# Kernel optimization log

Hardware: AMD Instinct MI355X
Metric: run time of the kernel (lower is better)

The kernel has to match this reference:

```python
import jax, jax.numpy as jnp
import numpy as np

N, K, FEAT = 64, 32, 1024      # nodes, neighbors per node, input feature dim
C1, F1 = 4, 16                 # layer1: out_channels=4, out_features=hidden[0]/4=16
C2, F2 = 32, 1                 # layer2: out_channels=hidden[1]=32, out_features=1
NUM_CLASS = 10
BN_EPS = 1e-5


def _sgnroot(x):
    return jnp.sign(x) * jnp.sqrt(jnp.clip(jnp.abs(x), 1e-8))


def _feature_adjacency(x, nb):
    # x: (N,c,f), nb: (N,K,c,f) -> adj: (N,c,f,f)
    fadj = jnp.einsum('nca,nkcb->ncab', x, nb)          # sum over K neighbors
    fadj = fadj + jnp.swapaxes(fadj, -2, -1)
    s = _sgnroot(fadj)
    out = s / (jnp.abs(s).sum(axis=1, keepdims=True) + 1e-7)  # row-normalize over channel dim
    return jnp.where(jnp.isnan(out), 0.0, out)


def _layer(x, nb, W, c_out, f_out):
    # FeatTrans1d.forward: adjacency build + batched matmul + full-width conv (== dense contraction)
    n = x.shape[0]
    adj = _feature_adjacency(x, nb)                     # (N,c,f,f)
    xa = jnp.einsum('ncab,ncb->nca', adj, x)            # adj @ x
    x2 = jnp.einsum('ocf,ncf->no', W, xa).reshape(n, c_out, f_out)
    na = jnp.einsum('ncab,nkcb->nkca', adj, nb)         # per-node adj applied to its neighbors
    nb2 = jnp.einsum('ocf,nkcf->nko', W, na).reshape(n, -1, c_out, f_out)
    return x2, nb2


def _bn_softsign_x(x, w, b):
    # BatchNorm1d (training stats over batch+feature dims) + Softsign; x: (N,C,F)
    m = x.mean(axis=(0, 2), keepdims=True)
    v = x.var(axis=(0, 2), keepdims=True)
    y = (x - m) / jnp.sqrt(v + BN_EPS) * w[None, :, None] + b[None, :, None]
    return y / (1.0 + jnp.abs(y))


def _bn_softsign_nb(x, w, b):
    # each node's neighbor set is normalized independently (list comprehension in original); x: (N,K,C,F)
    m = x.mean(axis=(1, 3), keepdims=True)
    v = x.var(axis=(1, 3), keepdims=True)
    y = (x - m) / jnp.sqrt(v + BN_EPS) * w[None, None, :, None] + b[None, None, :, None]
    return y / (1.0 + jnp.abs(y))


def setup_inputs() -> dict:
    key = jax.random.key(0)
    ks = jax.random.split(key, 6)
    return {
        'x': jax.random.normal(ks[0], (N, 1, FEAT), jnp.float32),
        'neighbor': jax.random.normal(ks[1], (N, K, 1, FEAT), jnp.float32),
        'W1': jax.random.normal(ks[2], (C1 * F1, 1, FEAT), jnp.float32) * (1.0 / FEAT) ** 0.5,
        'W2': jax.random.normal(ks[3], (C2 * F2, C1, F1), jnp.float32) * (1.0 / (C1 * F1)) ** 0.5,
        'bn1_w': jnp.ones((C1,), jnp.float32),
        'bn1_b': jnp.zeros((C1,), jnp.float32),
        'bn2_w': jnp.ones((C2,), jnp.float32),
        'bn2_b': jnp.zeros((C2,), jnp.float32),
        'lin_w': jax.random.normal(ks[4], (NUM_CLASS, C2 * F2), jnp.float32) * (1.0 / (C2 * F2)) ** 0.5,
        'lin_b': jnp.zeros((NUM_CLASS,), jnp.float32),
    }


def reference(x, neighbor, W1, W2, bn1_w, bn1_b, bn2_w, bn2_b, lin_w, lin_b):
    x1, nb1 = _layer(x, neighbor, W1, C1, F1)           # (N,4,16), (N,K,4,16)
    x1 = _bn_softsign_x(x1, bn1_w, bn1_b)
    nb1 = _bn_softsign_nb(nb1, bn1_w, bn1_b)
    x2, _ = _layer(x1, nb1, W2, C2, F2)                 # (N,32,1)
    x2 = _bn_softsign_x(x2, bn2_w, bn2_b)
    return x2.reshape(x2.shape[0], -1) @ lin_w.T + lin_b  # (N,NUM_CLASS)
```

## Files before the change

kernel.cpp:

```cpp
#include <hip/hip_runtime.h>

typedef unsigned short u16;
typedef short short8 __attribute__((ext_vector_type(8)));
typedef float floatx4 __attribute__((ext_vector_type(4)));
typedef float floatx2 __attribute__((ext_vector_type(2)));
typedef unsigned int uintx4 __attribute__((ext_vector_type(4)));
typedef unsigned int uintx2 __attribute__((ext_vector_type(2)));
typedef u16 ushortx4 __attribute__((ext_vector_type(4)));

#define FEAT 1024
#define KNB  32

__device__ __forceinline__ u16 f2bf(float f) {
    unsigned u = __float_as_uint(f);
    u += 0x7fffu + ((u >> 16) & 1u);
    return (u16)(u >> 16);
}
__device__ __forceinline__ unsigned pack2bf(float a, float b) {
    return (unsigned)f2bf(a) | ((unsigned)f2bf(b) << 16);
}
__device__ __forceinline__ float softsign(float v) { return v / (1.f + fabsf(v)); }

union Frag { uintx4 q; unsigned d[4]; short8 v; };

union SMem {
    struct {
        float sS[FEAT];
        float sX[FEAT];
        u16   sY[34 * 1024];
    } p1;
    struct {
        float sx2[64 * 64];
        float snb[32 * 64];
        float sx1[64], sS1[64], sadj[4 * 16 * 16], sxa[64];
        float ssc[4], sbi[4], ssc2[4], sbi2[4];
        int   flag;
    } p2;
    struct {
        float sy[64 * 32];
        float sx[64 * 32];
        float ssc[32], sbi[32];
    } p3;
};

__global__ __launch_bounds__(256, 2) void k_mega(
    const float* __restrict__ xg, const float* __restrict__ nbg,
    const float* __restrict__ w1g, const float* __restrict__ w2g,
    const float* __restrict__ bn1w, const float* __restrict__ bn1b,
    const float* __restrict__ bn2w, const float* __restrict__ bn2b,
    const float* __restrict__ linw, const float* __restrict__ linb,
    float* __restrict__ pws, float* __restrict__ x22ws,
    unsigned int* __restrict__ cnt, float* __restrict__ outg)
{
    __shared__ SMem sm;
    float* const sS = sm.p1.sS;
    float* const sX = sm.p1.sX;
    u16*   const sY = sm.p1.sY;

    const int t = threadIdx.x;
    const int bid = blockIdx.x;
    const int n = bid >> 3;
    const int chunk = bid & 7;
    const int chunkbase = chunk * 128;
    const int w = t >> 6;
    const int l = t & 63;
    const int m = l & 15;
    const int g = l >> 4;

    {
        ushortx4 z4 = {0, 0, 0, 0};
        *(ushortx4*)&sY[33 * 1024 + t * 4] = z4;
    }
    {
        floatx4 xv = *(const floatx4*)(xg + (size_t)n * FEAT + t * 4);
        *(floatx4*)&sX[t * 4] = xv;
        ushortx4 xb4 = {f2bf(xv[0]), f2bf(xv[1]), f2bf(xv[2]), f2bf(xv[3])};
        *(ushortx4*)&sY[t * 4] = xb4;
    }
    {
        const float* nbase = nbg + ((size_t)n * KNB) * FEAT + t * 4;
        floatx4 sacc = {0.f, 0.f, 0.f, 0.f};
        #pragma unroll 8
        for (int k = 0; k < KNB; ++k) {
            floatx4 v = *(const floatx4*)(nbase + (size_t)k * FEAT);
            sacc += v;
            int row = k + 1;
            int c16 = (t >> 1) ^ (row & 7);
            ushortx4 p4 = {f2bf(v[0]), f2bf(v[1]), f2bf(v[2]), f2bf(v[3])};
            *(ushortx4*)&sY[row * 1024 + c16 * 8 + (t & 1) * 4] = p4;
        }
        *(floatx4*)&sS[t * 4] = sacc;
    }

    const float xa0 = xg[(size_t)n * FEAT + chunkbase + w * 32 + m];
    const float xa1 = xg[(size_t)n * FEAT + chunkbase + w * 32 + 16 + m];
    __syncthreads();
    const float Sa0 = sS[chunkbase + w * 32 + m];
    const float Sa1 = sS[chunkbase + w * 32 + 16 + m];

    const u16* b2base = (m == 0) ? &sY[32 * 1024] : &sY[33 * 1024];
    const int sw = (m & 7);

    floatx4 acc[2][3];
    #pragma unroll
    for (int i = 0; i < 2; ++i)
        #pragma unroll
        for (int j = 0; j < 3; ++j) { floatx4 z = {0.f, 0.f, 0.f, 0.f}; acc[i][j] = z; }

    const floatx2 vxa0 = {xa0, xa0}, vxa1 = {xa1, xa1};
    const floatx2 vSa0 = {Sa0, Sa0}, vSa1 = {Sa1, Sa1};

    #pragma unroll 2
    for (int s = 0; s < 32; ++s) {
        const int bloc = s * 32 + g * 8;
        const int cidx = bloc >> 3;

        floatx4 xq0 = *(const floatx4*)&sX[bloc];
        floatx4 xq1 = *(const floatx4*)&sX[bloc + 4];
        floatx4 sq0 = *(const floatx4*)&sS[bloc];
        floatx4 sq1 = *(const floatx4*)&sS[bloc + 4];

        Frag af0, af1;
        #pragma unroll
        for (int p = 0; p < 4; ++p) {
            floatx2 xbp = (p < 2) ? ((p == 0) ? (floatx2){xq0[0], xq0[1]} : (floatx2){xq0[2], xq0[3]})
                                  : ((p == 2) ? (floatx2){xq1[0], xq1[1]} : (floatx2){xq1[2], xq1[3]});
            floatx2 sbp = (p < 2) ? ((p == 0) ? (floatx2){sq0[0], sq0[1]} : (floatx2){sq0[2], sq0[3]})
                                  : ((p == 2) ? (floatx2){sq1[0], sq1[1]} : (floatx2){sq1[2], sq1[3]});
            floatx2 u0 = xbp * vSa0 + sbp * vxa0;
            floatx2 u1 = xbp * vSa1 + sbp * vxa1;
            uintx2 b0b = __builtin_bit_cast(uintx2, u0);
            uintx2 b1b = __builtin_bit_cast(uintx2, u1);
            af0.d[p] = 0x3F803F80u | (b0b.y & 0x80000000u) | ((b0b.x >> 16) & 0x8000u);
            af1.d[p] = 0x3F803F80u | (b1b.y & 0x80000000u) | ((b1b.x >> 16) & 0x8000u);
        }

        Frag b0, b1, b2;
        b0.q = *(const uintx4*)&sY[ m       * 1024 + ((cidx ^ sw) << 3)];
        b1.q = *(const uintx4*)&sY[(16 + m) * 1024 + ((cidx ^ sw) << 3)];
        b2.q = *(const uintx4*)&b2base[cidx << 3];

        acc[0][0] = __builtin_amdgcn_mfma_f32_16x16x32_bf16(af0.v, b0.v, acc[0][0], 0, 0, 0);
        acc[0][1] = __builtin_amdgcn_mfma_f32_16x16x32_bf16(af0.v, b1.v, acc[0][1], 0, 0, 0);
        acc[0][2] = __builtin_amdgcn_mfma_f32_16x16x32_bf16(af0.v, b2.v, acc[0][2], 0, 0, 0);
        acc[1][0] = __builtin_amdgcn_mfma_f32_16x16x32_bf16(af1.v, b0.v, acc[1][0], 0, 0, 0);
        acc[1][1] = __builtin_amdgcn_mfma_f32_16x16x32_bf16(af1.v, b1.v, acc[1][1], 0, 0, 0);
        acc[1][2] = __builtin_amdgcn_mfma_f32_16x16x32_bf16(af1.v, b2.v, acc[1][2], 0, 0, 0);
    }
    __syncthreads();

    u16* sZ = sY;
    #pragma unroll
    for (int ti = 0; ti < 2; ++ti)
        #pragma unroll
        for (int jt = 0; jt < 3; ++jt) {
            int j = jt * 16 + m;
            int aloc = w * 32 + ti * 16 + g * 4;
            ushortx4 zz;
            zz.x = f2bf(acc[ti][jt][0]);
            zz.y = f2bf(acc[ti][jt][1]);
            zz.z = f2bf(acc[ti][jt][2]);
            zz.w = f2bf(acc[ti][jt][3]);
            *(ushortx4*)&sZ[j * 136 + aloc] = zz;
        }
    __syncthreads();

    floatx4 a2[3];
    #pragma unroll
    for (int j = 0; j < 3; ++j) { floatx4 z = {0.f, 0.f, 0.f, 0.f}; a2[j] = z; }
    #pragma unroll
    for (int kc = 0; kc < 4; ++kc) {
        const float* wsrc = w1g + (size_t)(w * 16 + m) * FEAT + chunkbase + kc * 32 + g * 8;
        floatx4 wf0 = *(const floatx4*)wsrc;
        floatx4 wf1 = *(const floatx4*)(wsrc + 4);
        Frag wb;
        wb.d[0] = pack2bf(wf0[0], wf0[1]);
        wb.d[1] = pack2bf(wf0[2], wf0[3]);
        wb.d[2] = pack2bf(wf1[0], wf1[1]);
        wb.d[3] = pack2bf(wf1[2], wf1[3]);
        #pragma unroll
        for (int jt = 0; jt < 3; ++jt) {
            Frag za;
            za.q = *(const uintx4*)&sZ[(jt * 16 + m) * 136 + kc * 32 + g * 8];
            a2[jt] = __builtin_amdgcn_mfma_f32_16x16x32_bf16(za.v, wb.v, a2[jt], 0, 0, 0);
        }
    }
    float* pbase = pws + (size_t)(n * 8 + chunk) * 33 * 64;
    #pragma unroll
    for (int jt = 0; jt < 3; ++jt)
        #pragma unroll
        for (int r = 0; r < 4; ++r) {
            int j = jt * 16 + g * 4 + r;
            if (j < 33)
                __hip_atomic_store(&pbase[j * 64 + w * 16 + m], a2[jt][r],
                                   __ATOMIC_RELAXED, __HIP_MEMORY_SCOPE_AGENT);
        }

    asm volatile("s_waitcnt vmcnt(0)" ::: "memory");
    __syncthreads();
    if (t == 0)
        __hip_atomic_fetch_add(&cnt[0], 1u, __ATOMIC_RELAXED, __HIP_MEMORY_SCOPE_AGENT);

    if ((bid & 7) != (n & 7)) return;

    if (t == 0) {
        while (__hip_atomic_load(&cnt[0], __ATOMIC_RELAXED, __HIP_MEMORY_SCOPE_AGENT) < 512u)
            __builtin_amdgcn_s_sleep(8);
    }
    __syncthreads();

    float* const sx2  = sm.p2.sx2;
    float* const snb  = sm.p2.snb;
    float* const sx1  = sm.p2.sx1;
    float* const sS1  = sm.p2.sS1;
    float* const sadj = sm.p2.sadj;
    float* const sxa  = sm.p2.sxa;
    float* const ssc  = sm.p2.ssc;
    float* const sbi  = sm.p2.sbi;
    float* const ssc2 = sm.p2.ssc2;
    float* const sbi2 = sm.p2.sbi2;

    #pragma unroll
    for (int r = 0; r < 4; ++r) {
        int slot = t + r * 256;
        int nn = slot >> 4, oc = slot & 15;
        const float* p = pws + (size_t)nn * 16896 + oc * 4;
        floatx4 tmp[8];
        #pragma unroll
        for (int c = 0; c < 8; ++c) tmp[c] = *(const floatx4*)(p + c * 2112);
        floatx4 s01 = tmp[0] + tmp[1], s23 = tmp[2] + tmp[3];
        floatx4 s45 = tmp[4] + tmp[5], s67 = tmp[6] + tmp[7];
        *(floatx4*)&sx2[slot * 4] = (s01 + s23) + (s45 + s67);
    }
    #pragma unroll
    for (int r = 0; r < 2; ++r) {
        int slot = t + r * 256;
        int k = slot >> 4, oc = slot & 15;
        const float* p = pws + (size_t)n * 16896 + (1 + k) * 64 + oc * 4;
        floatx4 tmp[8];
        #pragma unroll
        for (int c = 0; c < 8; ++c) tmp[c] = *(const floatx4*)(p + c * 2112);
        floatx4 s01 = tmp[0] + tmp[1], s23 = tmp[2] + tmp[3];
        floatx4 s45 = tmp[4] + tmp[5], s67 = tmp[6] + tmp[7];
        *(floatx4*)&snb[slot * 4] = (s01 + s23) + (s45 + s67);
    }
    __syncthreads();
    {
        int cc = t >> 6, l2 = t & 63;
        float s = 0.f, s2 = 0.f;
        #pragma unroll
        for (int i = 0; i < 16; ++i) {
            int idx = l2 * 16 + i;
            int nn = idx >> 4, f = idx & 15;
            float v = sx2[nn * 64 + cc * 16 + f];
            s += v; s2 += v * v;
        }
        float s3 = 0.f, s4 = 0.f;
        #pragma unroll
        for (int i = 0; i < 8; ++i) {
            int idx = l2 * 8 + i;
            int k = idx >> 4, f = idx & 15;
            float v = snb[k * 64 + cc * 16 + f];
            s3 += v; s4 += v * v;
        }
        #pragma unroll
        for (int off = 32; off > 0; off >>= 1) {
            s  += __shfl_down(s, off);  s2 += __shfl_down(s2, off);
            s3 += __shfl_down(s3, off); s4 += __shfl_down(s4, off);
        }
        if (l2 == 0) {
            float wv = bn1w[cc], bv = bn1b[cc];
            float mean = s * (1.f / 1024.f);
            float var = s2 * (1.f / 1024.f) - mean * mean;
            float rs = rsqrtf(var + 1e-5f);
            ssc[cc] = rs * wv;
            sbi[cc] = bv - mean * rs * wv;
            float mean2 = s3 * (1.f / 512.f);
            float var2 = s4 * (1.f / 512.f) - mean2 * mean2;
            float rs2 = rsqrtf(var2 + 1e-5f);
            ssc2[cc] = rs2 * wv;
            sbi2[cc] = bv - mean2 * rs2 * wv;
        }
    }
    __syncthreads();
    if (t < 64) {
        int cc = t >> 4;
        sx1[t] = softsign(sx2[n * 64 + t] * ssc[cc] + sbi[cc]);
        float a = 0.f;
        for (int k = 0; k < KNB; ++k)
            a += softsign(snb[k * 64 + t] * ssc2[cc] + sbi2[cc]);
        sS1[t] = a;
    }
    __syncthreads();
    {
        int a = t >> 4, b = t & 15;
        float sc[4]; float den = 1e-7f;
        #pragma unroll
        for (int c = 0; c < 4; ++c) {
            float u = sx1[c * 16 + a] * sS1[c * 16 + b] + sx1[c * 16 + b] * sS1[c * 16 + a];
            float r = sqrtf(fmaxf(fabsf(u), 1e-8f));
            sc[c] = copysignf(r, u);
            den += r;
        }
        float inv = 1.f / den;
        #pragma unroll
        for (int c = 0; c < 4; ++c) sadj[(c * 16 + a) * 16 + b] = sc[c] * inv;
    }
    __syncthreads();
    if (t < 64) {
        int cc = t >> 4;
        float a = 0.f;
        #pragma unroll
        for (int b = 0; b < 16; ++b) a += sadj[t * 16 + b] * sx1[cc * 16 + b];
        sxa[t] = a;
    }
    __syncthreads();
    if (t < 32) {
        float a = 0.f;
        #pragma unroll
        for (int cf = 0; cf < 64; ++cf) a += w2g[t * 64 + cf] * sxa[cf];
        __hip_atomic_store(&x22ws[n * 32 + t], a,
                           __ATOMIC_RELAXED, __HIP_MEMORY_SCOPE_AGENT);
    }

    asm volatile("s_waitcnt vmcnt(0)" ::: "memory");
    __syncthreads();
    if (t == 0)
        sm.p2.flag = (int)__hip_atomic_fetch_add(&cnt[1], 1u,
                        __ATOMIC_RELAXED, __HIP_MEMORY_SCOPE_AGENT);
    __syncthreads();
    if (sm.p2.flag != 63) return;

    float* const sy   = sm.p3.sy;
    float* const sx3  = sm.p3.sx;
    float* const ssc3 = sm.p3.ssc;
    float* const sbi3 = sm.p3.sbi;

    #pragma unroll
    for (int r = 0; r < 8; ++r) sx3[t + r * 256] = x22ws[t + r * 256];
    __syncthreads();
    if (t < 32) {
        float s = 0.f, s2 = 0.f;
        for (int nn = 0; nn < 64; ++nn) {
            float v = sx3[nn * 32 + t];
            s += v; s2 += v * v;
        }
        float mean = s * (1.f / 64.f);
        float var = s2 * (1.f / 64.f) - mean * mean;
        float rs = rsqrtf(var + 1e-5f);
        float wv = bn2w[t], bv = bn2b[t];
        ssc3[t] = rs * wv;
        sbi3[t] = bv - mean * rs * wv;
    }
    __syncthreads();
    #pragma unroll
    for (int r = 0; r < 8; ++r) {
        int idx = t + r * 256;
        int o = idx & 31;
        sy[idx] = softsign(sx3[idx] * ssc3[o] + sbi3[o]);
    }
    __syncthreads();
    for (int r = 0; r < 3; ++r) {
        int idx = t + r * 256;
        if (idx < 640) {
            int nn = idx / 10, cls = idx % 10;
            float a = linb[cls];
            #pragma unroll
            for (int o = 0; o < 32; ++o) a += sy[nn * 32 + o] * linw[cls * 32 + o];
            outg[idx] = a;
        }
    }
}

extern "C" void kernel_launch(void* const* d_in, const int* in_sizes, int n_in,
                              void* d_out, int out_size, void* d_ws, size_t ws_size,
                              hipStream_t stream) {
    (void)in_sizes; (void)n_in; (void)out_size; (void)ws_size;
    const float* xg   = (const float*)d_in[0];
    const float* nbg  = (const float*)d_in[1];
    const float* w1g  = (const float*)d_in[2];
    const float* w2g  = (const float*)d_in[3];
    const float* bn1w = (const float*)d_in[4];
    const float* bn1b = (const float*)d_in[5];
    const float* bn2w = (const float*)d_in[6];
    const float* bn2b = (const float*)d_in[7];
    const float* linw = (const float*)d_in[8];
    const float* linb = (const float*)d_in[9];

    float* pws   = (float*)d_ws;
    float* x22ws = pws + (size_t)64 * 8 * 33 * 64;
    unsigned int* cnt = (unsigned int*)(x22ws + 64 * 32);
    float* outg  = (float*)d_out;

    hipMemsetAsync(cnt, 0, 64, stream);
    k_mega<<<dim3(512), dim3(256), 0, stream>>>(xg, nbg, w1g, w2g, bn1w, bn1b,
                                                bn2w, bn2b, linw, linb,
                                                pws, x22ws, cnt, outg);
}
```

Measured before the change: 120.8 us.

## Split neighbor bf16 conversion across node's eight blocks and share via global workspace

Previously each of the 8 blocks per node redundantly loaded all 32 neighbor rows, converted them to bf16 and summed them. Now each block converts only 4 rows into a global bf16 buffer and writes a partial sum, then synchronizes with its sibling blocks through a per-node atomic counter spin-wait. Afterwards each block pulls the shared bf16 tile into LDS with direct global-to-LDS loads and reduces the 8 partial sums. This cuts redundant HBM reads and conversion work, but adds an inter-block barrier that depends on all 8 blocks being co-resident, plus an extra global round trip.

```diff
diff --git a/kernel.cpp b/kernel.cpp
--- a/kernel.cpp
+++ b/kernel.cpp
@@ -20,6 +20,12 @@
     return (unsigned)f2bf(a) | ((unsigned)f2bf(b) << 16);
 }
 __device__ __forceinline__ float softsign(float v) { return v / (1.f + fabsf(v)); }
+
+__device__ __forceinline__ void gload_lds16(const void* g, void* l) {
+    __builtin_amdgcn_global_load_lds(
+        (const __attribute__((address_space(1))) unsigned int*)g,
+        (__attribute__((address_space(3))) unsigned int*)l, 16, 0, 0);
+}
 
 union Frag { uintx4 q; unsigned d[4]; short8 v; };
 
@@ -50,7 +56,8 @@
     const float* __restrict__ bn2w, const float* __restrict__ bn2b,
     const float* __restrict__ linw, const float* __restrict__ linb,
     float* __restrict__ pws, float* __restrict__ x22ws,
-    unsigned int* __restrict__ cnt, float* __restrict__ outg)
+    unsigned int* __restrict__ cnt, u16* __restrict__ ybf,
+    float* __restrict__ spart, float* __restrict__ outg)
 {
     __shared__ SMem sm;
     float* const sS = sm.p1.sS;
@@ -68,28 +75,79 @@
     const int g = l >> 4;
 
     {
-        ushortx4 z4 = {0, 0, 0, 0};
-        *(ushortx4*)&sY[33 * 1024 + t * 4] = z4;
-    }
+        u16* yb = ybf + (size_t)n * 34816;
+        const int r0 = chunk * 4 + 1;
+        #pragma unroll
+        for (int p = 0; p < 2; ++p) {
+            int row = r0 + p * 2 + (t >> 7);
+            int cc = t & 127;
+            const float* src = nbg + (size_t)(n * KNB + row - 1) * FEAT + cc * 8;
+            floatx4 v0 = *(const floatx4*)src;
+            floatx4 v1 = *(const floatx4*)(src + 4);
+            unsigned long long lo = (unsigned long long)pack2bf(v0[0], v0[1])
+                                  | ((unsigned long long)pack2bf(v0[2], v0[3]) << 32);
+            unsigned long long hi = (unsigned long long)pack2bf(v1[0], v1[1])
+                                  | ((unsigned long long)pack2bf(v1[2], v1[3]) << 32);
+            unsigned long long* dst =
+                (unsigned long long*)&yb[row * 1024 + ((cc ^ (row & 7)) << 3)];
+            __hip_atomic_store(dst,     lo, __ATOMIC_RELAXED, __HIP_MEMORY_SCOPE_AGENT);
+            __hip_atomic_store(dst + 1, hi, __ATOMIC_RELAXED, __HIP_MEMORY_SCOPE_AGENT);
+        }
+        {
+            const float* sb = nbg + (size_t)(n * KNB + r0 - 1) * FEAT + t * 4;
+            floatx4 a = *(const floatx4*)sb;
+            floatx4 b = *(const floatx4*)(sb + FEAT);
+            floatx4 c2 = *(const floatx4*)(sb + 2 * FEAT);
+            floatx4 d = *(const floatx4*)(sb + 3 * FEAT);
+            floatx4 s4 = (a + b) + (c2 + d);
+            union { floatx4 f; unsigned long long q[2]; } u; u.f = s4;
+            unsigned long long* dst =
+                (unsigned long long*)&spart[(size_t)(n * 8 + chunk) * 1024 + t * 4];
+            __hip_atomic_store(dst,     u.q[0], __ATOMIC_RELAXED, __HIP_MEMORY_SCOPE_AGENT);
+            __hip_atomic_store(dst + 1, u.q[1], __ATOMIC_RELAXED, __HIP_MEMORY_SCOPE_AGENT);
+        }
+        if (chunk == 0 && t < 128) {
+            const float* src = xg + (size_t)n * FEAT + t * 8;
+            floatx4 v0 = *(const floatx4*)src;
+            floatx4 v1 = *(const floatx4*)(src + 4);
+            unsigned long long lo = (unsigned long long)pack2bf(v0[0], v0[1])
+                                  | ((unsigned long long)pack2bf(v0[2], v0[3]) << 32);
+            unsigned long long hi = (unsigned long long)pack2bf(v1[0], v1[1])
+                                  | ((unsigned long long)pack2bf(v1[2], v1[3]) << 32);
+            unsigned long long* dst = (unsigned long long*)&yb[t << 3];
+            __hip_atomic_store(dst,     lo, __ATOMIC_RELAXED, __HIP_MEMORY_SCOPE_AGENT);
+            __hip_atomic_store(dst + 1, hi, __ATOMIC_RELAXED, __HIP_MEMORY_SCOPE_AGENT);
+        }
+        if (chunk == 7 && t < 128) {
+            unsigned long long* dst = (unsigned long long*)&yb[33 * 1024 + (t << 3)];
+            __hip_atomic_store(dst,     0ull, __ATOMIC_RELAXED, __HIP_MEMORY_SCOPE_AGENT);
+            __hip_atomic_store(dst + 1, 0ull, __ATOMIC_RELAXED, __HIP_MEMORY_SCOPE_AGENT);
+        }
+        asm volatile("s_waitcnt vmcnt(0)" ::: "memory");
+        __syncthreads();
+        unsigned int* cN = &cnt[64 + n * 32];
+        if (t == 0) {
+            __hip_atomic_fetch_add(cN, 1u, __ATOMIC_RELAXED, __HIP_MEMORY_SCOPE_AGENT);
+            while (__hip_atomic_load(cN, __ATOMIC_RELAXED, __HIP_MEMORY_SCOPE_AGENT) < 8u)
+                __builtin_amdgcn_s_sleep(2);
+        }
+        __syncthreads();
+    }
+
     {
-        floatx4 xv = *(const floatx4*)(xg + (size_t)n * FEAT + t * 4);
-        *(floatx4*)&sX[t * 4] = xv;
-        ushortx4 xb4 = {f2bf(xv[0]), f2bf(xv[1]), f2bf(xv[2]), f2bf(xv[3])};
-        *(ushortx4*)&sY[t * 4] = xb4;
-    }
-    {
-        const float* nbase = nbg + ((size_t)n * KNB) * FEAT + t * 4;
-        floatx4 sacc = {0.f, 0.f, 0.f, 0.f};
-        #pragma unroll 8
-        for (int k = 0; k < KNB; ++k) {
-            floatx4 v = *(const floatx4*)(nbase + (size_t)k * FEAT);
-            sacc += v;
-            int row = k + 1;
-            int c16 = (t >> 1) ^ (row & 7);
-            ushortx4 p4 = {f2bf(v[0]), f2bf(v[1]), f2bf(v[2]), f2bf(v[3])};
-            *(ushortx4*)&sY[row * 1024 + c16 * 8 + (t & 1) * 4] = p4;
-        }
-        *(floatx4*)&sS[t * 4] = sacc;
+        const char* ysrc = (const char*)(ybf + (size_t)n * 34816);
+        char* ydst = (char*)sY;
+        #pragma unroll
+        for (int j2 = 0; j2 < 17; ++j2)
+            gload_lds16(ysrc + j2 * 4096 + w * 1024 + l * 16,
+                        ydst + j2 * 4096 + w * 1024);
+        gload_lds16((const char*)(xg + (size_t)n * FEAT) + w * 1024 + l * 16,
+                    (char*)sX + w * 1024);
+        const float* sp = spart + (size_t)n * 8192 + t * 4;
+        floatx4 a = {0.f, 0.f, 0.f, 0.f};
+        #pragma unroll
+        for (int c2 = 0; c2 < 8; ++c2) a += *(const floatx4*)(sp + c2 * 1024);
+        *(floatx4*)&sS[t * 4] = a;
     }
 
     const float xa0 = xg[(size_t)n * FEAT + chunkbase + w * 32 + m];
@@ -389,11 +447,13 @@
 
     float* pws   = (float*)d_ws;
     float* x22ws = pws + (size_t)64 * 8 * 33 * 64;
-    unsigned int* cnt = (unsigned int*)(x22ws + 64 * 32);
+    unsigned int* cnt = (unsigned int*)((char*)d_ws + 4333568);
+    u16* ybf     = (u16*)((char*)d_ws + 4349952);
+    float* spart = (float*)((char*)d_ws + 8806400);
     float* outg  = (float*)d_out;
 
-    hipMemsetAsync(cnt, 0, 64, stream);
+    hipMemsetAsync(cnt, 0, 16384, stream);
     k_mega<<<dim3(512), dim3(256), 0, stream>>>(xg, nbg, w1g, w2g, bn1w, bn1b,
                                                 bn2w, bn2b, linw, linb,
-                                                pws, x22ws, cnt, outg);
+                                                pws, x22ws, cnt, ybf, spart, outg);
 }
```

Measured after the change: 123.4 us. 2.2% more time.
